# Kernel tuning notes

Hardware: AMD Instinct MI355X
Metric: run time of the kernel (lower is better)

The kernel has to match this reference:

```python
import jax, jax.numpy as jnp
import numpy as np

C = 256
DK = C // 8  # query/key channels


def setup_inputs() -> dict:
    key = jax.random.key(0)
    ks = jax.random.split(key, 7)
    B, W, H = 4, 64, 64
    x = jax.random.normal(ks[0], (B, C, W, H), dtype=jnp.float32)
    s_in = 1.0 / np.sqrt(C)
    Wq = jax.random.normal(ks[1], (DK, C), dtype=jnp.float32) * s_in
    bq = jnp.zeros((DK,), dtype=jnp.float32)
    Wk = jax.random.normal(ks[2], (DK, C), dtype=jnp.float32) * s_in
    bk = jnp.zeros((DK,), dtype=jnp.float32)
    Wv = jax.random.normal(ks[3], (C, C), dtype=jnp.float32) * s_in
    bv = jnp.zeros((C,), dtype=jnp.float32)
    return {"x": x, "Wq": Wq, "bq": bq, "Wk": Wk, "bk": bk, "Wv": Wv, "bv": bv}


def reference(x, Wq, bq, Wk, bk, Wv, bv):
    B, Cc, W, H = x.shape
    N = W * H
    xf = x.reshape(B, Cc, N)  # (B, C, N) flattened spatial
    # 1x1 convs == channel matmuls
    q = jnp.einsum('dc,bcn->bnd', Wq, xf) + bq  # (B, N, DK)
    k = jnp.einsum('dc,bcn->bdn', Wk, xf) + bk[None, :, None]  # (B, DK, N)
    v = jnp.einsum('oc,bcn->bon', Wv, xf) + bv[None, :, None]  # (B, C, N)
    energy = jnp.einsum('bnd,bdm->bnm', q, k) / jnp.sqrt(jnp.float32(q.shape[-1]))
    attn = jax.nn.softmax(energy, axis=-1)  # (B, N, N)
    out = jnp.einsum('bcn,bmn->bcm', v, attn)  # v @ attn^T
    return out.reshape(B, Cc, W, H) + x
```

## Files before the change

### kernel.cpp

```cpp
#include <hip/hip_runtime.h>
#include <hip/hip_bf16.h>
#include <math.h>

#define BB 4
#define CC 256
#define DKK 32
#define NN 4096
#define QSCALE 0.2550181864060454f

typedef __attribute__((ext_vector_type(8))) __bf16 bf16x8;
typedef __attribute__((ext_vector_type(4))) __bf16 bf16x4;
typedef __attribute__((ext_vector_type(4))) float f32x4;

#define XST 260
#define SCRST 33

__global__ __launch_bounds__(256, 2) void qkv_kernel(
    const float* __restrict__ x,
    const float* __restrict__ Wq, const float* __restrict__ bq,
    const float* __restrict__ Wk, const float* __restrict__ bk,
    const float* __restrict__ Wv, const float* __restrict__ bv,
    __bf16* __restrict__ qws, __bf16* __restrict__ kws, __bf16* __restrict__ vws)
{
    __shared__ __align__(16) unsigned char smem[16640];
    __bf16* xsT = (__bf16*)smem;
    float*  scr = (float*)smem;

    const int tid = threadIdx.x;
    const int w   = tid >> 6;
    const int l   = tid & 63;
    const int l15 = l & 15;
    const int lq  = l >> 4;
    const int n0  = blockIdx.x * 32;
    const int b   = blockIdx.y;

    {
        const int cb = tid >> 3;
        const int nf = (tid & 7) * 4;
        const float* xp = x + ((size_t)(b * CC) + cb) * NN + n0 + nf;
#pragma unroll
        for (int r = 0; r < 8; r++) {
            float4 v = *(const float4*)(xp + (size_t)r * 32 * NN);
            int c = r * 32 + cb;
            xsT[(nf + 0) * XST + c] = (__bf16)v.x;
            xsT[(nf + 1) * XST + c] = (__bf16)v.y;
            xsT[(nf + 2) * XST + c] = (__bf16)v.z;
            xsT[(nf + 3) * XST + c] = (__bf16)v.w;
        }
    }

    const float* wp[5];
#pragma unroll
    for (int ot = 0; ot < 5; ot++) {
        int ob = 80 * w + 16 * ot;
        const float* src = (ob < 32) ? (Wq + (size_t)ob * CC)
                         : (ob < 64) ? (Wk + (size_t)(ob - 32) * CC)
                                     : (Wv + (size_t)(ob - 64) * CC);
        wp[ot] = src + (size_t)l15 * CC;
    }

    float4 wc[5][2], wn[5][2];
#pragma unroll
    for (int ot = 0; ot < 5; ot++) {
        wc[ot][0] = *(const float4*)(wp[ot] + lq * 8);
        wc[ot][1] = *(const float4*)(wp[ot] + lq * 8 + 4);
    }

    __syncthreads();

    const f32x4 zf = {0.f, 0.f, 0.f, 0.f};
    f32x4 acc[5][2];
#pragma unroll
    for (int i = 0; i < 5; i++)
#pragma unroll
        for (int j = 0; j < 2; j++) acc[i][j] = zf;

#pragma unroll
    for (int ks = 0; ks < 8; ks++) {
        if (ks < 7) {
#pragma unroll
            for (int ot = 0; ot < 5; ot++) {
                wn[ot][0] = *(const float4*)(wp[ot] + (ks + 1) * 32 + lq * 8);
                wn[ot][1] = *(const float4*)(wp[ot] + (ks + 1) * 32 + lq * 8 + 4);
            }
        }
        bf16x8 bfr[2];
#pragma unroll
        for (int nt = 0; nt < 2; nt++) {
            bf16x4 lo = *(const bf16x4*)&xsT[(nt * 16 + l15) * XST + ks * 32 + lq * 8];
            bf16x4 hi = *(const bf16x4*)&xsT[(nt * 16 + l15) * XST + ks * 32 + lq * 8 + 4];
            bfr[nt] = __builtin_shufflevector(lo, hi, 0, 1, 2, 3, 4, 5, 6, 7);
        }
#pragma unroll
        for (int ot = 0; ot < 5; ot++) {
            bf16x8 af;
            af[0] = (__bf16)wc[ot][0].x; af[1] = (__bf16)wc[ot][0].y;
            af[2] = (__bf16)wc[ot][0].z; af[3] = (__bf16)wc[ot][0].w;
            af[4] = (__bf16)wc[ot][1].x; af[5] = (__bf16)wc[ot][1].y;
            af[6] = (__bf16)wc[ot][1].z; af[7] = (__bf16)wc[ot][1].w;
#pragma unroll
            for (int nt = 0; nt < 2; nt++)
                acc[ot][nt] = __builtin_amdgcn_mfma_f32_16x16x32_bf16(af, bfr[nt], acc[ot][nt], 0, 0, 0);
        }
        if (ks < 7) {
#pragma unroll
            for (int ot = 0; ot < 5; ot++) { wc[ot][0] = wn[ot][0]; wc[ot][1] = wn[ot][1]; }
        }
    }

    __syncthreads();

    __bf16* vchunk = vws + (size_t)b * CC * NN + (size_t)(n0 >> 5) * 8192;
#pragma unroll
    for (int ot = 0; ot < 5; ot++) {
        int ob = 80 * w + ot * 16;
#pragma unroll
        for (int nt = 0; nt < 2; nt++) {
#pragma unroll
            for (int r = 0; r < 4; r++) {
                int o = ob + lq * 4 + r;
                int n = nt * 16 + l15;
                float val = acc[ot][nt][r];
                if (ob >= 64) {
                    int c = o - 64;
                    vchunk[(5 * w - 4 + ot) * 512 + (lq * 4 + r) * 32 + n] =
                        (__bf16)(val + bv[c]);
                } else if (ob < 32) {
                    scr[o * SCRST + n] = (val + bq[o]) * QSCALE;
                } else {
                    scr[o * SCRST + n] = val + bk[o - 32];
                }
            }
        }
    }
    __syncthreads();
    {
        int n  = tid >> 3;
        int d0 = (tid & 7) * 4;
        bf16x4 qv, kv;
#pragma unroll
        for (int j = 0; j < 4; j++) {
            qv[j] = (__bf16)scr[(d0 + j) * SCRST + n];
            kv[j] = (__bf16)scr[(32 + d0 + j) * SCRST + n];
        }
        size_t base = ((size_t)b * NN + n0 + n) * DKK + d0;
        *(bf16x4*)&qws[base] = qv;
        *(bf16x4*)&kws[base] = kv;
    }
}

#define PST 36
#define MST 68
#define PWSZ (64 * PST)

__global__ __launch_bounds__(256, 2) void attn_kernel(
    const __bf16* __restrict__ qb, const __bf16* __restrict__ kb,
    const __bf16* __restrict__ vt, const float* __restrict__ x,
    float* __restrict__ out)
{
    __shared__ __align__(16) unsigned char smem[38144];
    __bf16* pw   = (__bf16*)smem + (threadIdx.x >> 6) * 2 * PWSZ;
    float*  Ls   = (float*)(smem + 36864);
    float*  Linv = (float*)(smem + 37888);

    const int tid = threadIdx.x;
    const int w   = tid >> 6;
    const int l   = tid & 63;
    const int l15 = l & 15;
    const int lq  = l >> 4;

    const int beta = blockIdx.x;
    const int b    = (beta >> 1) & 3;
    const int ch   = (beta >> 3) & 1;
    const int mt   = ((beta >> 4) << 1) | (beta & 1);
    const int m0   = mt * 64;

    const __bf16* qbb = qb + (size_t)b * NN * DKK;
    const __bf16* kbb = kb + (size_t)b * NN * DKK;
    const __bf16* vtb = vt + (size_t)b * CC * NN;

    bf16x8 qa[4];
#pragma unroll
    for (int af = 0; af < 4; af++)
        qa[af] = *(const bf16x8*)(qbb + (size_t)(m0 + af * 16 + l15) * DKK + lq * 8);

    const __bf16* kstrip = kbb + (size_t)(w * 32 + l15) * DKK + lq * 8;
    const __bf16* vstrip = vtb + (size_t)w * 8192 + (size_t)ch * 4096
                               + l15 * 32 + lq * 8;

    const f32x4 zf = {0.f, 0.f, 0.f, 0.f};
    f32x4 acc[4][8];
#pragma unroll
    for (int i = 0; i < 4; i++)
#pragma unroll
        for (int j = 0; j < 8; j++) acc[i][j] = zf;
    float lacc[4] = {0.f, 0.f, 0.f, 0.f};

    bf16x8 kA0 = *(const bf16x8*)kstrip;
    bf16x8 kA1 = *(const bf16x8*)(kstrip + 16 * DKK);
#pragma unroll
    for (int af = 0; af < 4; af++) {
        f32x4 e0 = __builtin_amdgcn_mfma_f32_16x16x32_bf16(kA0, qa[af], zf, 0, 0, 0);
        f32x4 e1 = __builtin_amdgcn_mfma_f32_16x16x32_bf16(kA1, qa[af], zf, 0, 0, 0);
        bf16x4 p0, p1;
#pragma unroll
        for (int r = 0; r < 4; r++) {
            float v0 = __builtin_amdgcn_exp2f(e0[r]); lacc[af] += v0; p0[r] = (__bf16)v0;
            float v1 = __builtin_amdgcn_exp2f(e1[r]); lacc[af] += v1; p1[r] = (__bf16)v1;
        }
        *(bf16x4*)&pw[(af * 16 + l15) * PST + lq * 4]      = p0;
        *(bf16x4*)&pw[(af * 16 + l15) * PST + 16 + lq * 4] = p1;
    }
    kA0 = *(const bf16x8*)(kstrip + (size_t)128 * DKK);
    kA1 = *(const bf16x8*)(kstrip + (size_t)144 * DKK);

#pragma unroll 2
    for (int ic = 0; ic < 31; ic++) {
        const int cur = ic & 1;
        const __bf16* vch = vstrip + (size_t)ic * 32768;

        bf16x8 vfC[4], vfN[4];
#pragma unroll
        for (int ct = 0; ct < 4; ct++)
            vfC[ct] = *(const bf16x8*)(vch + ct * 512);

        bf16x8 pf[4];
#pragma unroll
        for (int af = 0; af < 4; af++) {
            bf16x4 plo = *(const bf16x4*)&pw[cur * PWSZ + (af * 16 + l15) * PST + lq * 8];
            bf16x4 phi = *(const bf16x4*)&pw[cur * PWSZ + (af * 16 + l15) * PST + lq * 8 + 4];
            pf[af] = __builtin_shufflevector(plo, phi, 0, 1, 2, 3, 4, 5, 6, 7);
        }

#pragma unroll
        for (int af = 0; af < 4; af++) {
            f32x4 e0 = __builtin_amdgcn_mfma_f32_16x16x32_bf16(kA0, qa[af], zf, 0, 0, 0);
            f32x4 e1 = __builtin_amdgcn_mfma_f32_16x16x32_bf16(kA1, qa[af], zf, 0, 0, 0);
            bf16x4 p0, p1;
#pragma unroll
            for (int r = 0; r < 4; r++) {
                float v0 = __builtin_amdgcn_exp2f(e0[r]); lacc[af] += v0; p0[r] = (__bf16)v0;
                float v1 = __builtin_amdgcn_exp2f(e1[r]); lacc[af] += v1; p1[r] = (__bf16)v1;
            }
            *(bf16x4*)&pw[(cur ^ 1) * PWSZ + (af * 16 + l15) * PST + lq * 4]      = p0;
            *(bf16x4*)&pw[(cur ^ 1) * PWSZ + (af * 16 + l15) * PST + 16 + lq * 4] = p1;
        }
        kA0 = *(const bf16x8*)(kstrip + (size_t)(ic + 2) * 128 * DKK);
        kA1 = *(const bf16x8*)(kstrip + (size_t)((ic + 2) * 128 + 16) * DKK);

#pragma unroll
        for (int ct = 0; ct < 4; ct++)
            vfN[ct] = *(const bf16x8*)(vch + (4 + ct) * 512);
#pragma unroll
        for (int ct = 0; ct < 4; ct++)
#pragma unroll
            for (int af = 0; af < 4; af++)
                acc[af][ct] = __builtin_amdgcn_mfma_f32_16x16x32_bf16(vfC[ct], pf[af], acc[af][ct], 0, 0, 0);
#pragma unroll
        for (int ct = 0; ct < 4; ct++)
#pragma unroll
            for (int af = 0; af < 4; af++)
                acc[af][4 + ct] = __builtin_amdgcn_mfma_f32_16x16x32_bf16(vfN[ct], pf[af], acc[af][4 + ct], 0, 0, 0);
    }

    {
        const __bf16* vch = vstrip + (size_t)31 * 32768;
        bf16x8 pf[4];
#pragma unroll
        for (int af = 0; af < 4; af++) {
            bf16x4 plo = *(const bf16x4*)&pw[(31 & 1) * PWSZ + (af * 16 + l15) * PST + lq * 8];
            bf16x4 phi = *(const bf16x4*)&pw[(31 & 1) * PWSZ + (af * 16 + l15) * PST + lq * 8 + 4];
            pf[af] = __builtin_shufflevector(plo, phi, 0, 1, 2, 3, 4, 5, 6, 7);
        }
        bf16x8 vfC[4], vfN[4];
#pragma unroll
        for (int ct = 0; ct < 4; ct++) vfC[ct] = *(const bf16x8*)(vch + ct * 512);
#pragma unroll
        for (int ct = 0; ct < 4; ct++) vfN[ct] = *(const bf16x8*)(vch + (4 + ct) * 512);
#pragma unroll
        for (int ct = 0; ct < 4; ct++)
#pragma unroll
            for (int af = 0; af < 4; af++)
                acc[af][ct] = __builtin_amdgcn_mfma_f32_16x16x32_bf16(vfC[ct], pf[af], acc[af][ct], 0, 0, 0);
#pragma unroll
        for (int ct = 0; ct < 4; ct++)
#pragma unroll
            for (int af = 0; af < 4; af++)
                acc[af][4 + ct] = __builtin_amdgcn_mfma_f32_16x16x32_bf16(vfN[ct], pf[af], acc[af][4 + ct], 0, 0, 0);
    }

#pragma unroll
    for (int af = 0; af < 4; af++) {
        lacc[af] += __shfl_xor(lacc[af], 16, 64);
        lacc[af] += __shfl_xor(lacc[af], 32, 64);
    }
    if (lq == 0) {
#pragma unroll
        for (int af = 0; af < 4; af++) Ls[w * 64 + af * 16 + l15] = lacc[af];
    }
    __syncthreads();
    if (tid < 64)
        Linv[tid] = 1.0f / (Ls[tid] + Ls[64 + tid] + Ls[128 + tid] + Ls[192 + tid]);

    float* Ored = (float*)smem + w * (32 * MST);
#pragma unroll
    for (int q = 0; q < 4; q++) {
        if (q > 0) __syncthreads();
#pragma unroll
        for (int ctp = 0; ctp < 2; ctp++) {
            int ct = 2 * q + ctp;
#pragma unroll
            for (int af = 0; af < 4; af++) {
#pragma unroll
                for (int r = 0; r < 4; r++)
                    Ored[(ctp * 16 + lq * 4 + r) * MST + af * 16 + l15] = acc[af][ct][r];
            }
        }
        __syncthreads();
        const int cl  = tid >> 3;
        const int mi0 = (tid & 7) * 8;
        const float* Ob = (const float*)smem + cl * MST;
#pragma unroll
        for (int j = 0; j < 2; j++) {
            int mi = mi0 + 4 * j;
            f32x4 s = *(const f32x4*)&Ob[mi];
            s = s + *(const f32x4*)&Ob[1 * (32 * MST) + mi];
            s = s + *(const f32x4*)&Ob[2 * (32 * MST) + mi];
            s = s + *(const f32x4*)&Ob[3 * (32 * MST) + mi];
            f32x4 li = *(const f32x4*)&Linv[mi];
            int c = ch * 128 + q * 32 + cl;
            size_t gi = ((size_t)(b * CC + c)) * NN + m0 + mi;
            f32x4 xr = *(const f32x4*)&x[gi];
            *(f32x4*)&out[gi] = s * li + xr;
        }
    }
}

extern "C" void kernel_launch(void* const* d_in, const int* in_sizes, int n_in,
                              void* d_out, int out_size, void* d_ws, size_t ws_size,
                              hipStream_t stream) {
    const float* x  = (const float*)d_in[0];
    const float* Wq = (const float*)d_in[1];
    const float* bq = (const float*)d_in[2];
    const float* Wk = (const float*)d_in[3];
    const float* bk = (const float*)d_in[4];
    const float* Wv = (const float*)d_in[5];
    const float* bv = (const float*)d_in[6];
    float* out = (float*)d_out;

    __bf16* qws = (__bf16*)d_ws;
    __bf16* kws = qws + (size_t)BB * NN * DKK;
    __bf16* vws = kws + (size_t)BB * NN * DKK;

    qkv_kernel<<<dim3(128, BB), 256, 0, stream>>>(x, Wq, bq, Wk, bk, Wv, bv,
                                                  qws, kws, vws);
    attn_kernel<<<dim3(512), 256, 0, stream>>>(qws, kws, vws, x, out);
}
```

Baseline: 153.1 us.

## Switch PV accumulation to 32x32x16 MFMA with matching V layout

Measured after the change: 152.5 us. About the same (-0.4%).

```diff
diff --git a/kernel.cpp b/kernel.cpp
--- a/kernel.cpp
+++ b/kernel.cpp
@@ -11,6 +11,7 @@
 typedef __attribute__((ext_vector_type(8))) __bf16 bf16x8;
 typedef __attribute__((ext_vector_type(4))) __bf16 bf16x4;
 typedef __attribute__((ext_vector_type(4))) float f32x4;
+typedef __attribute__((ext_vector_type(16))) float f32x16;
 
 #define XST 260
 #define SCRST 33
@@ -123,7 +124,7 @@
                 float val = acc[ot][nt][r];
                 if (ob >= 64) {
                     int c = o - 64;
-                    vchunk[(5 * w - 4 + ot) * 512 + (lq * 4 + r) * 32 + n] =
+                    vchunk[(c >> 5) * 1024 + nt * 512 + (c & 31) * 16 + l15] =
                         (__bf16)(val + bv[c]);
                 } else if (ob < 32) {
                     scr[o * SCRST + n] = (val + bq[o]) * QSCALE;
@@ -168,6 +169,8 @@
     const int l   = tid & 63;
     const int l15 = l & 15;
     const int lq  = l >> 4;
+    const int l31 = l & 31;
+    const int lh  = l >> 5;
 
     const int beta = blockIdx.x;
     const int b    = (beta >> 1) & 3;
@@ -186,14 +189,18 @@
 
     const __bf16* kstrip = kbb + (size_t)(w * 32 + l15) * DKK + lq * 8;
     const __bf16* vstrip = vtb + (size_t)w * 8192 + (size_t)ch * 4096
-                               + l15 * 32 + lq * 8;
-
-    const f32x4 zf = {0.f, 0.f, 0.f, 0.f};
-    f32x4 acc[4][8];
-#pragma unroll
-    for (int i = 0; i < 4; i++)
-#pragma unroll
-        for (int j = 0; j < 8; j++) acc[i][j] = zf;
+                               + l31 * 16 + lh * 8;
+
+    const f32x4  zf  = {0.f, 0.f, 0.f, 0.f};
+    f32x16 acc32[2][4];
+    {
+        const f32x16 z16 = {0.f,0.f,0.f,0.f,0.f,0.f,0.f,0.f,
+                            0.f,0.f,0.f,0.f,0.f,0.f,0.f,0.f};
+#pragma unroll
+        for (int i = 0; i < 2; i++)
+#pragma unroll
+            for (int j = 0; j < 4; j++) acc32[i][j] = z16;
+    }
     float lacc[4] = {0.f, 0.f, 0.f, 0.f};
 
     bf16x8 kA0 = *(const bf16x8*)kstrip;
@@ -219,18 +226,23 @@
         const int cur = ic & 1;
         const __bf16* vch = vstrip + (size_t)ic * 32768;
 
-        bf16x8 vfC[4], vfN[4];
-#pragma unroll
-        for (int ct = 0; ct < 4; ct++)
-            vfC[ct] = *(const bf16x8*)(vch + ct * 512);
-
-        bf16x8 pf[4];
-#pragma unroll
-        for (int af = 0; af < 4; af++) {
-            bf16x4 plo = *(const bf16x4*)&pw[cur * PWSZ + (af * 16 + l15) * PST + lq * 8];
-            bf16x4 phi = *(const bf16x4*)&pw[cur * PWSZ + (af * 16 + l15) * PST + lq * 8 + 4];
-            pf[af] = __builtin_shufflevector(plo, phi, 0, 1, 2, 3, 4, 5, 6, 7);
-        }
+        bf16x8 vf[4][2];
+#pragma unroll
+        for (int ct = 0; ct < 4; ct++) {
+            vf[ct][0] = *(const bf16x8*)(vch + ct * 1024);
+            vf[ct][1] = *(const bf16x8*)(vch + ct * 1024 + 512);
+        }
+
+        bf16x8 pf[2][2];
+#pragma unroll
+        for (int mt2 = 0; mt2 < 2; mt2++)
+#pragma unroll
+            for (int ks = 0; ks < 2; ks++) {
+                const __bf16* pr = &pw[cur * PWSZ + (mt2 * 32 + l31) * PST + ks * 16 + lh * 8];
+                bf16x4 plo = *(const bf16x4*)pr;
+                bf16x4 phi = *(const bf16x4*)(pr + 4);
+                pf[mt2][ks] = __builtin_shufflevector(plo, phi, 0, 1, 2, 3, 4, 5, 6, 7);
+            }
 
 #pragma unroll
         for (int af = 0; af < 4; af++) {
@@ -249,44 +261,43 @@
         kA1 = *(const bf16x8*)(kstrip + (size_t)((ic + 2) * 128 + 16) * DKK);
 
 #pragma unroll
-        for (int ct = 0; ct < 4; ct++)
-            vfN[ct] = *(const bf16x8*)(vch + (4 + ct) * 512);
-#pragma unroll
-        for (int ct = 0; ct < 4; ct++)
-#pragma unroll
-            for (int af = 0; af < 4; af++)
-                acc[af][ct] = __builtin_amdgcn_mfma_f32_16x16x32_bf16(vfC[ct], pf[af], acc[af][ct], 0, 0, 0);
-#pragma unroll
-        for (int ct = 0; ct < 4; ct++)
-#pragma unroll
-            for (int af = 0; af < 4; af++)
-                acc[af][4 + ct] = __builtin_amdgcn_mfma_f32_16x16x32_bf16(vfN[ct], pf[af], acc[af][4 + ct], 0, 0, 0);
+        for (int mt2 = 0; mt2 < 2; mt2++)
+#pragma unroll
+            for (int ct = 0; ct < 4; ct++) {
+                acc32[mt2][ct] = __builtin_amdgcn_mfma_f32_32x32x16_bf16(
+                    vf[ct][0], pf[mt2][0], acc32[mt2][ct], 0, 0, 0);
+                acc32[mt2][ct] = __builtin_amdgcn_mfma_f32_32x32x16_bf16(
+                    vf[ct][1], pf[mt2][1], acc32[mt2][ct], 0, 0, 0);
+            }
     }
 
     {
         const __bf16* vch = vstrip + (size_t)31 * 32768;
-        bf16x8 pf[4];
-#pragma unroll
-        for (int af = 0; af < 4; af++) {
-            bf16x4 plo = *(const bf16x4*)&pw[(31 & 1) * PWSZ + (af * 16 + l15) * PST + lq * 8];
-            bf16x4 phi = *(const bf16x4*)&pw[(31 & 1) * PWSZ + (af * 16 + l15) * PST + lq * 8 + 4];
-            pf[af] = __builtin_shufflevector(plo, phi, 0, 1, 2, 3, 4, 5, 6, 7);
-        }
-        bf16x8 vfC[4], vfN[4];
-#pragma unroll
-        for (int ct = 0; ct < 4; ct++) vfC[ct] = *(const bf16x8*)(vch + ct * 512);
-#pragma unroll
-        for (int ct = 0; ct < 4; ct++) vfN[ct] = *(const bf16x8*)(vch + (4 + ct) * 512);
-#pragma unroll
-        for (int ct = 0; ct < 4; ct++)
-#pragma unroll
-            for (int af = 0; af < 4; af++)
-                acc[af][ct] = __builtin_amdgcn_mfma_f32_16x16x32_bf16(vfC[ct], pf[af], acc[af][ct], 0, 0, 0);
-#pragma unroll
-        for (int ct = 0; ct < 4; ct++)
-#pragma unroll
-            for (int af = 0; af < 4; af++)
-                acc[af][4 + ct] = __builtin_amdgcn_mfma_f32_16x16x32_bf16(vfN[ct], pf[af], acc[af][4 + ct], 0, 0, 0);
+        bf16x8 vf[4][2];
+#pragma unroll
+        for (int ct = 0; ct < 4; ct++) {
+            vf[ct][0] = *(const bf16x8*)(vch + ct * 1024);
+            vf[ct][1] = *(const bf16x8*)(vch + ct * 1024 + 512);
+        }
+        bf16x8 pf[2][2];
+#pragma unroll
+        for (int mt2 = 0; mt2 < 2; mt2++)
+#pragma unroll
+            for (int ks = 0; ks < 2; ks++) {
+                const __bf16* pr = &pw[(31 & 1) * PWSZ + (mt2 * 32 + l31) * PST + ks * 16 + lh * 8];
+                bf16x4 plo = *(const bf16x4*)pr;
+                bf16x4 phi = *(const bf16x4*)(pr + 4);
+                pf[mt2][ks] = __builtin_shufflevector(plo, phi, 0, 1, 2, 3, 4, 5, 6, 7);
+            }
+#pragma unroll
+        for (int mt2 = 0; mt2 < 2; mt2++)
+#pragma unroll
+            for (int ct = 0; ct < 4; ct++) {
+                acc32[mt2][ct] = __builtin_amdgcn_mfma_f32_32x32x16_bf16(
+                    vf[ct][0], pf[mt2][0], acc32[mt2][ct], 0, 0, 0);
+                acc32[mt2][ct] = __builtin_amdgcn_mfma_f32_32x32x16_bf16(
+                    vf[ct][1], pf[mt2][1], acc32[mt2][ct], 0, 0, 0);
+            }
     }
 
 #pragma unroll
@@ -307,13 +318,11 @@
     for (int q = 0; q < 4; q++) {
         if (q > 0) __syncthreads();
 #pragma unroll
-        for (int ctp = 0; ctp < 2; ctp++) {
-            int ct = 2 * q + ctp;
-#pragma unroll
-            for (int af = 0; af < 4; af++) {
-#pragma unroll
-                for (int r = 0; r < 4; r++)
-                    Ored[(ctp * 16 + lq * 4 + r) * MST + af * 16 + l15] = acc[af][ct][r];
+        for (int mt2 = 0; mt2 < 2; mt2++) {
+#pragma unroll
+            for (int reg = 0; reg < 16; reg++) {
+                int row = (reg & 3) + 8 * (reg >> 2) + 4 * lh;
+                Ored[row * MST + mt2 * 32 + l31] = acc32[mt2][q][reg];
             }
         }
         __syncthreads();
```
